# Kernel tuning notes

Hardware: AMD Instinct MI355X
Metric: run time of the kernel (lower is better)

Reference implementation:

```python
import jax, jax.numpy as jnp
import numpy as np

EPS = 1e-6

def rms_norm(x, w, eps=EPS):
    # x: [B, L, C]; matches WanRMSNorm: x * rsqrt(mean(x^2) + eps) * weight
    v = jnp.mean(x * x, axis=-1, keepdims=True)
    return x * jax.lax.rsqrt(v + eps) * w

def rope_apply(x, grid_sizes, freqs):
    # x: [B, L, n, d]; freqs: [1024, d//2] angles (original passes e^{i*ang})
    B, L, n, d = x.shape
    c = d // 2
    c1 = c // 3
    c0 = c - 2 * c1
    f0, f1, f2 = freqs[:, :c0], freqs[:, c0:c0 + c1], freqs[:, c0 + c1:]
    gs = np.asarray(grid_sizes)  # concrete per-sample grid sizes (ragged loop)
    outs = []
    for i in range(B):
        f, h, w = int(gs[i, 0]), int(gs[i, 1]), int(gs[i, 2])
        sl = f * h * w
        ang = jnp.concatenate([
            jnp.broadcast_to(f0[:f][:, None, None, :], (f, h, w, c0)),
            jnp.broadcast_to(f1[:h][None, :, None, :], (f, h, w, c1)),
            jnp.broadcast_to(f2[:w][None, None, :, :], (f, h, w, c1)),
        ], axis=-1).reshape(sl, 1, c)
        xi = x[i, :sl].reshape(sl, n, c, 2)  # consecutive pairs = complex (re, im)
        re, im = xi[..., 0], xi[..., 1]
        cs, sn = jnp.cos(ang), jnp.sin(ang)
        rot = jnp.stack([re * cs - im * sn, re * sn + im * cs], axis=-1).reshape(sl, n, d)
        outs.append(jnp.concatenate([rot, x[i, sl:]], axis=0))
    return jnp.stack(outs).astype(jnp.float32)

def attention(q, k, v, seq_lens):
    # full (window_size=(-1,-1)) attention with key-length masking (k_lens)
    B, L, n, d = q.shape
    scale = 1.0 / jnp.sqrt(jnp.asarray(d, jnp.float32))
    scores = jnp.einsum('bqnd,bknd->bnqk', q, k) * scale
    kmask = jnp.arange(L)[None, :] < seq_lens[:, None]  # [B, L]
    scores = jnp.where(kmask[:, None, None, :], scores, jnp.asarray(-1e30, scores.dtype))
    p = jax.nn.softmax(scores, axis=-1)
    return jnp.einsum('bnqk,bknd->bqnd', p, v)


def setup_inputs() -> dict:
    key = jax.random.key(0)
    ks = jax.random.split(key, 8)
    B, L, dim, n = 1, 5000, 1536, 12
    d = dim // n           # 128
    c = d // 2             # 64
    c1 = c // 3            # 21
    c0 = c - 2 * c1        # 22

    x = jax.random.normal(ks[0], (B, L, dim), jnp.float32)
    grid_sizes = jnp.asarray([[8, 25, 25]], jnp.int32)  # F*H*W = 5000 = L
    seq_lens = jnp.full((B,), L, jnp.int32)

    # RoPE angles: pos * base^{-j/size} per (f, h, w) component
    pos = jnp.arange(1024, dtype=jnp.float32)[:, None]
    def comp(sz):
        return pos * (10000.0 ** (-jnp.arange(sz, dtype=jnp.float32) / sz))
    freqs = jnp.concatenate([comp(c0), comp(c1), comp(c1)], axis=1)  # [1024, 64]

    def lin(k):
        return jax.random.normal(k, (dim, dim), jnp.float32) * 0.02
    return {
        'x': x, 'seq_lens': seq_lens, 'grid_sizes': grid_sizes, 'freqs': freqs,
        'Wq': lin(ks[1]), 'bq': jnp.zeros((dim,), jnp.float32),
        'Wk': lin(ks[2]), 'bk': jnp.zeros((dim,), jnp.float32),
        'Wv': lin(ks[3]), 'bv': jnp.zeros((dim,), jnp.float32),
        'Wo': lin(ks[4]), 'bo': jnp.zeros((dim,), jnp.float32),
        'gq': jnp.ones((dim,), jnp.float32),
        'gk': jnp.ones((dim,), jnp.float32),
    }


def reference(x, seq_lens, grid_sizes, freqs, Wq, bq, Wk, bk, Wv, bv, Wo, bo, gq, gk):
    B, L, dim = x.shape
    d = 2 * freqs.shape[1]
    n = dim // d
    q = rms_norm(x @ Wq + bq, gq).reshape(B, L, n, d)
    k = rms_norm(x @ Wk + bk, gk).reshape(B, L, n, d)
    v = (x @ Wv + bv).reshape(B, L, n, d)
    q = rope_apply(q, grid_sizes, freqs)
    k = rope_apply(k, grid_sizes, freqs)
    o = attention(q, k, v, seq_lens)          # [B, L, n, d]
    return o.reshape(B, L, dim) @ Wo + bo
```

## Files before the change

kernel.cpp:

```cpp
#include <hip/hip_runtime.h>

typedef unsigned short u16;
typedef unsigned int   u32;
typedef short bf16x8 __attribute__((ext_vector_type(8)));
typedef float f32x4  __attribute__((ext_vector_type(4)));

__device__ __forceinline__ float b2f(u16 u){ return __uint_as_float(((u32)u) << 16); }
__device__ __forceinline__ u16 f2bf(float f){
  u32 u = __float_as_uint(f);
  return (u16)((u + 0x7fffu + ((u >> 16) & 1u)) >> 16);
}

__global__ __launch_bounds__(256) void transpose4(
    const float* __restrict__ Wq, const float* __restrict__ Wk,
    const float* __restrict__ Wv, const float* __restrict__ Wo, u16* __restrict__ wt)
{
  __shared__ float tile[32][33];
  const float* src = blockIdx.z == 0 ? Wq : blockIdx.z == 1 ? Wk : blockIdx.z == 2 ? Wv : Wo;
  u16* dst = wt + (size_t)blockIdx.z * 1536 * 1536;
  const int bx = blockIdx.x * 32, by = blockIdx.y * 32;
  const int tx = threadIdx.x, ty = threadIdx.y;
#pragma unroll
  for (int i = 0; i < 32; i += 8)
    tile[ty + i][tx] = src[(size_t)(by + ty + i) * 1536 + bx + tx];
  __syncthreads();
#pragma unroll
  for (int i = 0; i < 32; i += 8)
    dst[(size_t)(bx + ty + i) * 1536 + by + tx] = f2bf(tile[tx][ty + i]);
}

__global__ __launch_bounds__(256) void cast_f32_bf16(
    const float* __restrict__ src, u16* __restrict__ dst, int n4)
{
  int i = blockIdx.x * 256 + threadIdx.x;
  if (i < n4) {
    float4 f = ((const float4*)src)[i];
    ushort4 o;
    o.x = f2bf(f.x); o.y = f2bf(f.y); o.z = f2bf(f.z); o.w = f2bf(f.w);
    ((ushort4*)dst)[i] = o;
  }
}

__global__ __launch_bounds__(256) void transpose_v(
    const u16* __restrict__ src, u16* __restrict__ dst, int L, int Lpad)
{
  __shared__ u16 tile[64][72];
  const int kb = blockIdx.x * 64, c0 = blockIdx.y * 64;
  const int tid = threadIdx.x;
#pragma unroll
  for (int i = 0; i < 2; i++) {
    int slot = tid + i * 256;
    int row = slot >> 3, oct = slot & 7;
    bf16x8 z = {0, 0, 0, 0, 0, 0, 0, 0};
    int key = kb + row;
    if (key < L) z = *(const bf16x8*)(src + (size_t)key * 1536 + c0 + oct * 8);
    *(bf16x8*)&tile[row][oct * 8] = z;
  }
  __syncthreads();
#pragma unroll
  for (int i = 0; i < 2; i++) {
    int slot = tid + i * 256;
    int d = slot >> 3, oct = slot & 7;
    bf16x8 z;
#pragma unroll
    for (int j = 0; j < 8; j++) z[j] = (short)tile[oct * 8 + j][d];
    *(bf16x8*)(dst + (size_t)(c0 + d) * Lpad + kb + oct * 8) = z;
  }
}

template<bool F32OUT>
__device__ __forceinline__ void gemm_core(
    const u16* __restrict__ A, const u16* __restrict__ BT,
    const float* __restrict__ bias, void* __restrict__ Cv, int M,
    int m0, int n0)
{
  __shared__ u16 As[128][40];
  __shared__ u16 Bs[128][40];
  const int tid = threadIdx.x;
  const int wave = tid >> 6, lane = tid & 63;
  const int wm = (wave & 1) * 64, wn = (wave >> 1) * 64;
  const int l16 = lane & 15, quad = lane >> 4;
  f32x4 acc[4][4] = {};
  for (int k0 = 0; k0 < 1536; k0 += 32) {
    __syncthreads();
#pragma unroll
    for (int i = 0; i < 2; i++) {
      int c = tid + i * 256;
      int row = c >> 2, col = (c & 3) * 8;
      bf16x8 av = {0, 0, 0, 0, 0, 0, 0, 0};
      int gr = m0 + row;
      if (gr < M) av = *(const bf16x8*)(A + (size_t)gr * 1536 + k0 + col);
      *(bf16x8*)&As[row][col] = av;
      *(bf16x8*)&Bs[row][col] = *(const bf16x8*)(BT + (size_t)(n0 + row) * 1536 + k0 + col);
    }
    __syncthreads();
    bf16x8 af[4], bfr[4];
#pragma unroll
    for (int mt = 0; mt < 4; mt++) af[mt] = *(const bf16x8*)&As[wm + mt * 16 + l16][quad * 8];
#pragma unroll
    for (int nt = 0; nt < 4; nt++) bfr[nt] = *(const bf16x8*)&Bs[wn + nt * 16 + l16][quad * 8];
#pragma unroll
    for (int mt = 0; mt < 4; mt++)
#pragma unroll
      for (int nt = 0; nt < 4; nt++)
        acc[mt][nt] = __builtin_amdgcn_mfma_f32_16x16x32_bf16(af[mt], bfr[nt], acc[mt][nt], 0, 0, 0);
  }
#pragma unroll
  for (int nt = 0; nt < 4; nt++) {
    int col = n0 + wn + nt * 16 + l16;
    float bv = bias[col];
#pragma unroll
    for (int mt = 0; mt < 4; mt++) {
      int rowb = m0 + wm + mt * 16 + quad * 4;
#pragma unroll
      for (int r = 0; r < 4; r++) {
        int row = rowb + r;
        if (row < M) {
          float val = acc[mt][nt][r] + bv;
          if (F32OUT) ((float*)Cv)[(size_t)row * 1536 + col] = val;
          else        ((u16*)Cv)[(size_t)row * 1536 + col] = f2bf(val);
        }
      }
    }
  }
}

__global__ __launch_bounds__(256) void gemm_qkv(
    const u16* __restrict__ A, const u16* __restrict__ wt,
    const float* __restrict__ bq, const float* __restrict__ bk, const float* __restrict__ bv,
    u16* __restrict__ outbase, int M, size_t SZW, size_t SZT)
{
  const int z = blockIdx.z;
  const u16* BT = wt + (size_t)z * SZW;
  const float* bias = z == 0 ? bq : z == 1 ? bk : bv;
  u16* C = outbase + (size_t)z * SZT;
  gemm_core<false>(A, BT, bias, C, M, blockIdx.x * 128, blockIdx.y * 128);
}

__global__ __launch_bounds__(256) void gemm_out(
    const u16* __restrict__ A, const u16* __restrict__ BT,
    const float* __restrict__ bias, float* __restrict__ C, int M)
{
  gemm_core<true>(A, BT, bias, C, M, blockIdx.x * 128, blockIdx.y * 128);
}

__global__ __launch_bounds__(256) void rmsrope(
    u16* __restrict__ qb, u16* __restrict__ kb,
    const float* __restrict__ gq, const float* __restrict__ gk,
    const float* __restrict__ freqs, const int* __restrict__ gsz)
{
  const int s = blockIdx.x, tid = threadIdx.x;
  const size_t base = (size_t)s * 1536;
  float qv[6], kv[6];
  float sq = 0.f, sk = 0.f;
#pragma unroll
  for (int i = 0; i < 6; i++) {
    float a = b2f(qb[base + tid * 6 + i]); qv[i] = a; sq += a * a;
    float b = b2f(kb[base + tid * 6 + i]); kv[i] = b; sk += b * b;
  }
#pragma unroll
  for (int d2 = 1; d2 < 64; d2 <<= 1) { sq += __shfl_xor(sq, d2); sk += __shfl_xor(sk, d2); }
  __shared__ float red[8];
  const int wave = tid >> 6, lane = tid & 63;
  if (lane == 0) { red[wave] = sq; red[4 + wave] = sk; }
  __syncthreads();
  sq = red[0] + red[1] + red[2] + red[3];
  sk = red[4] + red[5] + red[6] + red[7];
  const float rq = rsqrtf(sq * (1.f / 1536.f) + 1e-6f);
  const float rk = rsqrtf(sk * (1.f / 1536.f) + 1e-6f);
  const int F = gsz[0], H = gsz[1], W = gsz[2];
  const int sl = F * H * W;
  const bool rope = s < sl;
  int pf = 0, ph = 0, pw = 0;
  if (rope) { pf = s / (H * W); int rr = s - pf * (H * W); ph = rr / W; pw = rr - ph * W; }
#pragma unroll
  for (int pp = 0; pp < 3; pp++) {
    const int j0 = tid * 6 + pp * 2;
    float qre = qv[pp * 2]     * rq * gq[j0];
    float qim = qv[pp * 2 + 1] * rq * gq[j0 + 1];
    float kre = kv[pp * 2]     * rk * gk[j0];
    float kim = kv[pp * 2 + 1] * rk * gk[j0 + 1];
    if (rope) {
      const int ti = (j0 & 127) >> 1;
      const int pos = ti < 22 ? pf : (ti < 43 ? ph : pw);
      const float ang = freqs[pos * 64 + ti];
      const float cs = cosf(ang), sn = sinf(ang);
      float t1 = qre * cs - qim * sn; qim = qre * sn + qim * cs; qre = t1;
      float t2 = kre * cs - kim * sn; kim = kre * sn + kim * cs; kre = t2;
    }
    qb[base + j0] = f2bf(qre); qb[base + j0 + 1] = f2bf(qim);
    kb[base + j0] = f2bf(kre); kb[base + j0 + 1] = f2bf(kim);
  }
}

__global__ __launch_bounds__(256, 2) void attn_mfma(
    const u16* __restrict__ q, const u16* __restrict__ k, const u16* __restrict__ vt,
    u16* __restrict__ o, const int* __restrict__ seq_lens, int L, int Lpad)
{
  __shared__ u16 Ks[64][136];
  __shared__ u16 Vs[128][72];
  __shared__ u16 Pl[4][32][72];
  const int tid = threadIdx.x, wave = tid >> 6, lane = tid & 63;
  const int l16 = lane & 15, quad = lane >> 4;
  const int h = blockIdx.y;
  const int seqlen = seq_lens[0];
  const int q0 = blockIdx.x * 128 + wave * 32;
  const float SC = 0.12752551286084934f;

  int krow[4], kcol[4], vd[4], voct[4];
#pragma unroll
  for (int i = 0; i < 4; i++) {
    int slot = tid + i * 256;
    krow[i] = slot >> 4; kcol[i] = (slot & 15) * 8;
    vd[i]   = slot >> 3; voct[i] = (slot & 7) * 8;
  }
  const u16* kp  = k + h * 128;
  const u16* vtp = vt + (size_t)h * 128 * Lpad;

  bf16x8 Qf[2][4];
#pragma unroll
  for (int qg = 0; qg < 2; qg++) {
    int qr = q0 + qg * 16 + l16;
#pragma unroll
    for (int ds = 0; ds < 4; ds++) {
      bf16x8 z = {0, 0, 0, 0, 0, 0, 0, 0};
      if (qr < L) {
        bf16x8 raw = *(const bf16x8*)(q + (size_t)qr * 1536 + h * 128 + ds * 32 + quad * 8);
#pragma unroll
        for (int j = 0; j < 8; j++) z[j] = (short)f2bf(b2f((u16)raw[j]) * SC);
      }
      Qf[qg][ds] = z;
    }
  }
  f32x4 accO[2][8] = {};
  float m_i[2] = {-1e30f, -1e30f}, l_i[2] = {0.f, 0.f};

  const int ntile = (seqlen + 63) >> 6;
  bf16x8 kpre[4], vpre[4];
#pragma unroll
  for (int i = 0; i < 4; i++) {
    int row = krow[i];
    bf16x8 z = {0, 0, 0, 0, 0, 0, 0, 0};
    if (row < seqlen) z = *(const bf16x8*)(kp + (size_t)row * 1536 + kcol[i]);
    kpre[i] = z;
    vpre[i] = *(const bf16x8*)(vtp + (size_t)vd[i] * Lpad + voct[i]);
  }

  for (int t = 0; t < ntile; t++) {
    const int kb = t * 64;
    __syncthreads();
#pragma unroll
    for (int i = 0; i < 4; i++) {
      *(bf16x8*)&Ks[krow[i]][kcol[i]] = kpre[i];
      *(bf16x8*)&Vs[vd[i]][voct[i]]   = vpre[i];
    }
    __syncthreads();
    if (t + 1 < ntile) {
      const int kb2 = kb + 64;
#pragma unroll
      for (int i = 0; i < 4; i++) {
        int row = kb2 + krow[i];
        bf16x8 z = {0, 0, 0, 0, 0, 0, 0, 0};
        if (row < seqlen) z = *(const bf16x8*)(kp + (size_t)row * 1536 + kcol[i]);
        kpre[i] = z;
        vpre[i] = *(const bf16x8*)(vtp + (size_t)vd[i] * Lpad + kb2 + voct[i]);
      }
    }

    const bool full = (kb + 64 <= seqlen);
    float sv[2][16];
    float tmax[2] = {-1e30f, -1e30f};
#pragma unroll
    for (int kt = 0; kt < 4; kt++) {
      f32x4 a0 = {0.f, 0.f, 0.f, 0.f};
      f32x4 a1 = {0.f, 0.f, 0.f, 0.f};
#pragma unroll
      for (int ds = 0; ds < 4; ds++) {
        bf16x8 kf = *(const bf16x8*)&Ks[kt * 16 + l16][ds * 32 + quad * 8];
        a0 = __builtin_amdgcn_mfma_f32_16x16x32_bf16(kf, Qf[0][ds], a0, 0, 0, 0);
        a1 = __builtin_amdgcn_mfma_f32_16x16x32_bf16(kf, Qf[1][ds], a1, 0, 0, 0);
      }
      if (full) {
#pragma unroll
        for (int r = 0; r < 4; r++) {
          sv[0][kt * 4 + r] = a0[r]; tmax[0] = fmaxf(tmax[0], a0[r]);
          sv[1][kt * 4 + r] = a1[r]; tmax[1] = fmaxf(tmax[1], a1[r]);
        }
      } else {
#pragma unroll
        for (int r = 0; r < 4; r++) {
          int key = kb + kt * 16 + quad * 4 + r;
          float s0 = (key < seqlen) ? a0[r] : -1e30f;
          float s1 = (key < seqlen) ? a1[r] : -1e30f;
          sv[0][kt * 4 + r] = s0; tmax[0] = fmaxf(tmax[0], s0);
          sv[1][kt * 4 + r] = s1; tmax[1] = fmaxf(tmax[1], s1);
        }
      }
    }
    float alpha[2];
#pragma unroll
    for (int qg = 0; qg < 2; qg++) {
      float tm = tmax[qg];
      tm = fmaxf(tm, __shfl_xor(tm, 16));
      tm = fmaxf(tm, __shfl_xor(tm, 32));
      const float mnew = fmaxf(m_i[qg], tm);
      alpha[qg] = exp2f(m_i[qg] - mnew);
      float psum = 0.f;
      u16 pk[16];
#pragma unroll
      for (int i2 = 0; i2 < 16; i2++) {
        float p = exp2f(sv[qg][i2] - mnew);
        u32 pu = __float_as_uint(p) & 0xffff0000u;
        psum += __uint_as_float(pu);
        pk[i2] = (u16)(pu >> 16);
      }
      psum += __shfl_xor(psum, 16);
      psum += __shfl_xor(psum, 32);
      l_i[qg] = l_i[qg] * alpha[qg] + psum;
      m_i[qg] = mnew;
#pragma unroll
      for (int kt = 0; kt < 4; kt++) {
        ushort4 w4 = { pk[kt * 4], pk[kt * 4 + 1], pk[kt * 4 + 2], pk[kt * 4 + 3] };
        *(ushort4*)&Pl[wave][qg * 16 + l16][kt * 16 + quad * 4] = w4;
      }
    }
#pragma unroll
    for (int qg = 0; qg < 2; qg++) {
      float ar[4];
#pragma unroll
      for (int r = 0; r < 4; r++) ar[r] = __shfl(alpha[qg], quad * 4 + r);
#pragma unroll
      for (int dt = 0; dt < 8; dt++)
#pragma unroll
        for (int r = 0; r < 4; r++) accO[qg][dt][r] *= ar[r];
    }
    bf16x8 pf00 = *(const bf16x8*)&Pl[wave][l16][quad * 8];
    bf16x8 pf01 = *(const bf16x8*)&Pl[wave][l16][32 + quad * 8];
    bf16x8 pf10 = *(const bf16x8*)&Pl[wave][16 + l16][quad * 8];
    bf16x8 pf11 = *(const bf16x8*)&Pl[wave][16 + l16][32 + quad * 8];
#pragma unroll
    for (int dt = 0; dt < 8; dt++) {
      bf16x8 vf0 = *(const bf16x8*)&Vs[dt * 16 + l16][quad * 8];
      bf16x8 vf1 = *(const bf16x8*)&Vs[dt * 16 + l16][32 + quad * 8];
      accO[0][dt] = __builtin_amdgcn_mfma_f32_16x16x32_bf16(pf00, vf0, accO[0][dt], 0, 0, 0);
      accO[0][dt] = __builtin_amdgcn_mfma_f32_16x16x32_bf16(pf01, vf1, accO[0][dt], 0, 0, 0);
      accO[1][dt] = __builtin_amdgcn_mfma_f32_16x16x32_bf16(pf10, vf0, accO[1][dt], 0, 0, 0);
      accO[1][dt] = __builtin_amdgcn_mfma_f32_16x16x32_bf16(pf11, vf1, accO[1][dt], 0, 0, 0);
    }
  }
#pragma unroll
  for (int qg = 0; qg < 2; qg++) {
    float linv[4];
#pragma unroll
    for (int r = 0; r < 4; r++) linv[r] = 1.f / __shfl(l_i[qg], quad * 4 + r);
#pragma unroll
    for (int r = 0; r < 4; r++) {
      int qr = q0 + qg * 16 + quad * 4 + r;
      if (qr < L) {
#pragma unroll
        for (int dt = 0; dt < 8; dt++)
          o[(size_t)qr * 1536 + h * 128 + dt * 16 + l16] = f2bf(accO[qg][dt][r] * linv[r]);
      }
    }
  }
}

extern "C" void kernel_launch(void* const* d_in, const int* in_sizes, int n_in,
                              void* d_out, int out_size, void* d_ws, size_t ws_size,
                              hipStream_t stream) {
  const float* x      = (const float*)d_in[0];
  const int* seq_lens = (const int*)d_in[1];
  const int* gsz      = (const int*)d_in[2];
  const float* freqs  = (const float*)d_in[3];
  const float* Wq     = (const float*)d_in[4];
  const float* bq     = (const float*)d_in[5];
  const float* Wk     = (const float*)d_in[6];
  const float* bk     = (const float*)d_in[7];
  const float* Wv     = (const float*)d_in[8];
  const float* bv     = (const float*)d_in[9];
  const float* Wo     = (const float*)d_in[10];
  const float* bo     = (const float*)d_in[11];
  const float* gq     = (const float*)d_in[12];
  const float* gk     = (const float*)d_in[13];
  float* out = (float*)d_out;

  const int DIM = 1536;
  const int L = in_sizes[0] / DIM;
  const int Lpad = ((L + 63) / 64) * 64;
  const size_t SZW = (size_t)DIM * DIM;
  const size_t SZT = (size_t)L * DIM;

  u16* wt   = (u16*)d_ws;
  u16* xb   = wt + 4 * SZW;
  u16* qraw = xb + SZT;
  u16* kraw = qraw + SZT;
  u16* vraw = kraw + SZT;
  u16* vtb  = vraw + SZT;
  u16* attn = vtb + (size_t)DIM * Lpad;

  const int mtiles = (L + 127) / 128;

  transpose4<<<dim3(48, 48, 4), dim3(32, 8), 0, stream>>>(Wq, Wk, Wv, Wo, wt);
  cast_f32_bf16<<<(int)((SZT / 4 + 255) / 256), 256, 0, stream>>>(x, xb, (int)(SZT / 4));
  gemm_qkv<<<dim3(mtiles, 12, 3), 256, 0, stream>>>(xb, wt, bq, bk, bv, qraw, L, SZW, SZT);
  rmsrope<<<dim3(L), 256, 0, stream>>>(qraw, kraw, gq, gk, freqs, gsz);
  transpose_v<<<dim3((L + 63) / 64, DIM / 64), 256, 0, stream>>>(vraw, vtb, L, Lpad);
  attn_mfma<<<dim3((L + 127) / 128, 12), 256, 0, stream>>>(qraw, kraw, vtb, attn, seq_lens, L, Lpad);
  gemm_out<<<dim3(mtiles, 12), 256, 0, stream>>>(attn, wt + 3 * SZW, bo, out, L);
}
```

Measured before the change: 607.6 us.

## Double-buffer GEMM tiles via direct global-to-LDS loads and lazily rescale attention

```diff
diff --git a/kernel.cpp b/kernel.cpp
--- a/kernel.cpp
+++ b/kernel.cpp
@@ -9,6 +9,12 @@
 __device__ __forceinline__ u16 f2bf(float f){
   u32 u = __float_as_uint(f);
   return (u16)((u + 0x7fffu + ((u >> 16) & 1u)) >> 16);
+}
+
+__device__ __forceinline__ void gload16(const u16* g, u16* l) {
+  __builtin_amdgcn_global_load_lds(
+      (const __attribute__((address_space(1))) unsigned int*)(g),
+      (__attribute__((address_space(3))) unsigned int*)(l), 16, 0, 0);
 }
 
 __global__ __launch_bounds__(256) void transpose4(
@@ -74,37 +80,52 @@
     const float* __restrict__ bias, void* __restrict__ Cv, int M,
     int m0, int n0)
 {
-  __shared__ u16 As[128][40];
-  __shared__ u16 Bs[128][40];
+  __shared__ u16 As[2][128][32];
+  __shared__ u16 Bs[2][128][32];
   const int tid = threadIdx.x;
   const int wave = tid >> 6, lane = tid & 63;
   const int wm = (wave & 1) * 64, wn = (wave >> 1) * 64;
   const int l16 = lane & 15, quad = lane >> 4;
+
+  const int srow = lane >> 2, scol = (lane & 3) * 8;
+  const u16* ap0 = A  + (size_t)(m0 + wave * 32 + srow) * 1536 + scol;
+  const u16* ap1 = ap0 + (size_t)16 * 1536;
+  const u16* bp0 = BT + (size_t)(n0 + wave * 32 + srow) * 1536 + scol;
+  const u16* bp1 = bp0 + (size_t)16 * 1536;
+
+#define STAGE_GEMM(curb) do { \
+    gload16(ap0, &As[curb][wave * 32][0]); \
+    gload16(ap1, &As[curb][wave * 32 + 16][0]); \
+    gload16(bp0, &Bs[curb][wave * 32][0]); \
+    gload16(bp1, &Bs[curb][wave * 32 + 16][0]); \
+    ap0 += 32; ap1 += 32; bp0 += 32; bp1 += 32; } while (0)
+
   f32x4 acc[4][4] = {};
-  for (int k0 = 0; k0 < 1536; k0 += 32) {
-    __syncthreads();
-#pragma unroll
-    for (int i = 0; i < 2; i++) {
-      int c = tid + i * 256;
-      int row = c >> 2, col = (c & 3) * 8;
-      bf16x8 av = {0, 0, 0, 0, 0, 0, 0, 0};
-      int gr = m0 + row;
-      if (gr < M) av = *(const bf16x8*)(A + (size_t)gr * 1536 + k0 + col);
-      *(bf16x8*)&As[row][col] = av;
-      *(bf16x8*)&Bs[row][col] = *(const bf16x8*)(BT + (size_t)(n0 + row) * 1536 + k0 + col);
-    }
-    __syncthreads();
+  STAGE_GEMM(0);
+  for (int ks = 0; ks < 48; ks++) {
+    const int cur = ks & 1;
+    if (ks + 1 < 48) {
+      STAGE_GEMM(cur ^ 1);
+      asm volatile("s_waitcnt vmcnt(4)" ::: "memory");
+    } else {
+      asm volatile("s_waitcnt vmcnt(0)" ::: "memory");
+    }
+    __builtin_amdgcn_s_barrier();
+    __builtin_amdgcn_sched_barrier(0);
     bf16x8 af[4], bfr[4];
 #pragma unroll
-    for (int mt = 0; mt < 4; mt++) af[mt] = *(const bf16x8*)&As[wm + mt * 16 + l16][quad * 8];
-#pragma unroll
-    for (int nt = 0; nt < 4; nt++) bfr[nt] = *(const bf16x8*)&Bs[wn + nt * 16 + l16][quad * 8];
+    for (int mt = 0; mt < 4; mt++) af[mt] = *(const bf16x8*)&As[cur][wm + mt * 16 + l16][quad * 8];
+#pragma unroll
+    for (int nt = 0; nt < 4; nt++) bfr[nt] = *(const bf16x8*)&Bs[cur][wn + nt * 16 + l16][quad * 8];
 #pragma unroll
     for (int mt = 0; mt < 4; mt++)
 #pragma unroll
       for (int nt = 0; nt < 4; nt++)
         acc[mt][nt] = __builtin_amdgcn_mfma_f32_16x16x32_bf16(af[mt], bfr[nt], acc[mt][nt], 0, 0, 0);
-  }
+    __builtin_amdgcn_s_barrier();
+  }
+#undef STAGE_GEMM
+
 #pragma unroll
   for (int nt = 0; nt < 4; nt++) {
     int col = n0 + wn + nt * 16 + l16;
@@ -297,14 +318,19 @@
         }
       }
     }
-    float alpha[2];
+    float alpha[2] = {1.f, 1.f};
+    bool resc[2];
 #pragma unroll
     for (int qg = 0; qg < 2; qg++) {
       float tm = tmax[qg];
       tm = fmaxf(tm, __shfl_xor(tm, 16));
       tm = fmaxf(tm, __shfl_xor(tm, 32));
-      const float mnew = fmaxf(m_i[qg], tm);
-      alpha[qg] = exp2f(m_i[qg] - mnew);
+      resc[qg] = !__all(tm - m_i[qg] <= 8.f);
+      float mnew = m_i[qg];
+      if (resc[qg]) {
+        mnew = fmaxf(m_i[qg], tm);
+        alpha[qg] = exp2f(m_i[qg] - mnew);
+      }
       float psum = 0.f;
       u16 pk[16];
 #pragma unroll
@@ -316,7 +342,7 @@
       }
       psum += __shfl_xor(psum, 16);
       psum += __shfl_xor(psum, 32);
-      l_i[qg] = l_i[qg] * alpha[qg] + psum;
+      l_i[qg] = (resc[qg] ? l_i[qg] * alpha[qg] : l_i[qg]) + psum;
       m_i[qg] = mnew;
 #pragma unroll
       for (int kt = 0; kt < 4; kt++) {
@@ -326,13 +352,15 @@
     }
 #pragma unroll
     for (int qg = 0; qg < 2; qg++) {
-      float ar[4];
-#pragma unroll
-      for (int r = 0; r < 4; r++) ar[r] = __shfl(alpha[qg], quad * 4 + r);
-#pragma unroll
-      for (int dt = 0; dt < 8; dt++)
-#pragma unroll
-        for (int r = 0; r < 4; r++) accO[qg][dt][r] *= ar[r];
+      if (resc[qg]) {
+        float ar[4];
+#pragma unroll
+        for (int r = 0; r < 4; r++) ar[r] = __shfl(alpha[qg], quad * 4 + r);
+#pragma unroll
+        for (int dt = 0; dt < 8; dt++)
+#pragma unroll
+          for (int r = 0; r < 4; r++) accO[qg][dt][r] *= ar[r];
+      }
     }
     bf16x8 pf00 = *(const bf16x8*)&Pl[wave][l16][quad * 8];
     bf16x8 pf01 = *(const bf16x8*)&Pl[wave][l16][32 + quad * 8];
@@ -392,11 +420,11 @@
 
   u16* wt   = (u16*)d_ws;
   u16* xb   = wt + 4 * SZW;
-  u16* qraw = xb + SZT;
+  u16* attn = xb + SZT;
+  u16* qraw = attn + SZT;
   u16* kraw = qraw + SZT;
   u16* vraw = kraw + SZT;
   u16* vtb  = vraw + SZT;
-  u16* attn = vtb + (size_t)DIM * Lpad;
 
   const int mtiles = (L + 127) / 128;
 
```

Measured after the change: 557.7 us. 1.09x faster.
